# Optimization experiments

Hardware: AMD Instinct MI355X
Metric: run time of the kernel (lower is better)

The kernel has to match this reference:

```python
import jax, jax.numpy as jnp
import numpy as np

K = 1000   # grid rows (detections from model 1, truncated to 1000)
N = 1000   # grid cols (detections from model 2)
M = 900000 # number of non-empty (overlapping) pairs
F = 7      # per-pair feature dim
SENTINEL = -9999.0


def setup_inputs() -> dict:
    key = jax.random.key(0)
    ks = jax.random.split(key, 12)
    def w(k, o, i):
        return jax.random.normal(k, (o, i), dtype=jnp.float32) * 0.05
    def b(k, o):
        return jax.random.normal(k, (o,), dtype=jnp.float32) * 0.05
    return {
        "input_1": jax.random.normal(ks[0], (1, F, 1, M), dtype=jnp.float32),
        "T_out": jnp.zeros((1, K, N), dtype=jnp.float32),
        "T_indices": jax.random.randint(ks[1], (2, M), 0, K),
        "w1": w(ks[2], 18, F),  "b1": b(ks[3], 18),
        "w2": w(ks[4], 36, 18), "b2": b(ks[5], 36),
        "w3": w(ks[6], 36, 36), "b3": b(ks[7], 36),
        "w4": w(ks[8], 1, 36),  "b4": b(ks[9], 1),
    }


def reference(input_1, T_out, T_indices, w1, b1, w2, b2, w3, b3, w4, b4):
    # 1x1 conv stack == channel matmuls on the flattened [F, M] features.
    x = input_1[0, :, 0, :]                       # [F, M]
    h = jax.nn.relu(w1 @ x + b1[:, None])         # [18, M]
    h = jax.nn.relu(w2 @ h + b2[:, None])         # [36, M]
    h = jax.nn.relu(w3 @ h + b3[:, None])         # [36, M]
    vals = (w4 @ h + b4[:, None])[0]              # [M]

    grid = jnp.full(T_out.shape, SENTINEL, dtype=T_out.dtype)  # [1, K, N]
    grid = grid.at[:, T_indices[0], T_indices[1]].set(vals[None, :])

    # MaxPool2d([1, N]) -> max over cols; MaxPool2d([K, 1]) -> max over rows.
    row_max = grid.max(axis=2).squeeze()          # [K]
    col_max = grid.max(axis=1).squeeze()          # [N]
    return (row_max, col_max)
```

## Files before the change

### kernel.cpp

```cpp
#include <hip/hip_runtime.h>
#include <stdint.h>

#define KK 1000
#define NN 1000
#define MM 900000
#define FF 7
#define SENTINEL -9999.0f

#define R18(X) X(0) X(1) X(2) X(3) X(4) X(5) X(6) X(7) X(8) X(9) X(10) X(11) \
               X(12) X(13) X(14) X(15) X(16) X(17)
#define R36(X) R18(X) X(18) X(19) X(20) X(21) X(22) X(23) X(24) X(25) X(26) \
               X(27) X(28) X(29) X(30) X(31) X(32) X(33) X(34) X(35)

__global__ __launch_bounds__(256) void init_grid(ulonglong2* __restrict__ g, int n2) {
    int i = blockIdx.x * 256 + threadIdx.x;
    if (i < n2) g[i] = make_ulonglong2(0ULL, 0ULL);
}

__global__ __launch_bounds__(256, 4) void mlp_scatter(
    const float* __restrict__ in,
    const int*   __restrict__ idx,
    const float* __restrict__ w1, const float* __restrict__ b1,
    const float* __restrict__ w2, const float* __restrict__ b2,
    const float* __restrict__ w3, const float* __restrict__ b3,
    const float* __restrict__ w4, const float* __restrict__ b4,
    unsigned long long* __restrict__ grid)
{
    int m0 = blockIdx.x * 256 + threadIdx.x;
    int m = m0 < MM ? m0 : (MM - 1);

    float x0 = in[0 * MM + m], x1 = in[1 * MM + m], x2 = in[2 * MM + m],
          x3 = in[3 * MM + m], x4 = in[4 * MM + m], x5 = in[5 * MM + m],
          x6 = in[6 * MM + m];

#define L1(o) float h1_##o; { float a = b1[o];                                 \
    a = fmaf(w1[(o)*7+0], x0, a); a = fmaf(w1[(o)*7+1], x1, a);                \
    a = fmaf(w1[(o)*7+2], x2, a); a = fmaf(w1[(o)*7+3], x3, a);                \
    a = fmaf(w1[(o)*7+4], x4, a); a = fmaf(w1[(o)*7+5], x5, a);                \
    a = fmaf(w1[(o)*7+6], x6, a); h1_##o = fmaxf(a, 0.0f); }
    R18(L1)
#undef L1

#define L2(o) float h2_##o; { float a = b2[o];                                 \
    a = fmaf(w2[(o)*18+ 0], h1_0,  a); a = fmaf(w2[(o)*18+ 1], h1_1,  a);      \
    a = fmaf(w2[(o)*18+ 2], h1_2,  a); a = fmaf(w2[(o)*18+ 3], h1_3,  a);      \
    a = fmaf(w2[(o)*18+ 4], h1_4,  a); a = fmaf(w2[(o)*18+ 5], h1_5,  a);      \
    a = fmaf(w2[(o)*18+ 6], h1_6,  a); a = fmaf(w2[(o)*18+ 7], h1_7,  a);      \
    a = fmaf(w2[(o)*18+ 8], h1_8,  a); a = fmaf(w2[(o)*18+ 9], h1_9,  a);      \
    a = fmaf(w2[(o)*18+10], h1_10, a); a = fmaf(w2[(o)*18+11], h1_11, a);      \
    a = fmaf(w2[(o)*18+12], h1_12, a); a = fmaf(w2[(o)*18+13], h1_13, a);      \
    a = fmaf(w2[(o)*18+14], h1_14, a); a = fmaf(w2[(o)*18+15], h1_15, a);      \
    a = fmaf(w2[(o)*18+16], h1_16, a); a = fmaf(w2[(o)*18+17], h1_17, a);      \
    h2_##o = fmaxf(a, 0.0f); }
    R36(L2)
#undef L2

    float v = b4[0];
#define L34(o) { float a = b3[o];                                              \
    a = fmaf(w3[(o)*36+ 0], h2_0,  a); a = fmaf(w3[(o)*36+ 1], h2_1,  a);      \
    a = fmaf(w3[(o)*36+ 2], h2_2,  a); a = fmaf(w3[(o)*36+ 3], h2_3,  a);      \
    a = fmaf(w3[(o)*36+ 4], h2_4,  a); a = fmaf(w3[(o)*36+ 5], h2_5,  a);      \
    a = fmaf(w3[(o)*36+ 6], h2_6,  a); a = fmaf(w3[(o)*36+ 7], h2_7,  a);      \
    a = fmaf(w3[(o)*36+ 8], h2_8,  a); a = fmaf(w3[(o)*36+ 9], h2_9,  a);      \
    a = fmaf(w3[(o)*36+10], h2_10, a); a = fmaf(w3[(o)*36+11], h2_11, a);      \
    a = fmaf(w3[(o)*36+12], h2_12, a); a = fmaf(w3[(o)*36+13], h2_13, a);      \
    a = fmaf(w3[(o)*36+14], h2_14, a); a = fmaf(w3[(o)*36+15], h2_15, a);      \
    a = fmaf(w3[(o)*36+16], h2_16, a); a = fmaf(w3[(o)*36+17], h2_17, a);      \
    a = fmaf(w3[(o)*36+18], h2_18, a); a = fmaf(w3[(o)*36+19], h2_19, a);      \
    a = fmaf(w3[(o)*36+20], h2_20, a); a = fmaf(w3[(o)*36+21], h2_21, a);      \
    a = fmaf(w3[(o)*36+22], h2_22, a); a = fmaf(w3[(o)*36+23], h2_23, a);      \
    a = fmaf(w3[(o)*36+24], h2_24, a); a = fmaf(w3[(o)*36+25], h2_25, a);      \
    a = fmaf(w3[(o)*36+26], h2_26, a); a = fmaf(w3[(o)*36+27], h2_27, a);      \
    a = fmaf(w3[(o)*36+28], h2_28, a); a = fmaf(w3[(o)*36+29], h2_29, a);      \
    a = fmaf(w3[(o)*36+30], h2_30, a); a = fmaf(w3[(o)*36+31], h2_31, a);      \
    a = fmaf(w3[(o)*36+32], h2_32, a); a = fmaf(w3[(o)*36+33], h2_33, a);      \
    a = fmaf(w3[(o)*36+34], h2_34, a); a = fmaf(w3[(o)*36+35], h2_35, a);      \
    v = fmaf(w4[o], fmaxf(a, 0.0f), v); }
    R36(L34)
#undef L34

    int r = idx[m];
    int c = idx[MM + m];
    unsigned long long packed =
        ((unsigned long long)(unsigned)(m + 1) << 32) | (unsigned)__float_as_uint(v);
    atomicMax(&grid[r * NN + c], packed);
}

__global__ __launch_bounds__(256) void row_max_k(const unsigned long long* __restrict__ g,
                                                 float* __restrict__ out) {
    int r = blockIdx.x;
    float mx = SENTINEL;
    for (int c = threadIdx.x; c < NN; c += 256) {
        unsigned long long p = g[(size_t)r * NN + c];
        if (p) mx = fmaxf(mx, __uint_as_float((unsigned)p));
    }
    __shared__ float red[256];
    red[threadIdx.x] = mx;
    __syncthreads();
    for (int s = 128; s > 0; s >>= 1) {
        if (threadIdx.x < s) red[threadIdx.x] = fmaxf(red[threadIdx.x], red[threadIdx.x + s]);
        __syncthreads();
    }
    if (threadIdx.x == 0) out[r] = red[0];
}

#define CCHUNKS 25
#define CROWS   (KK / CCHUNKS)

__global__ __launch_bounds__(256) void col_partial(const unsigned long long* __restrict__ g,
                                                   float* __restrict__ part) {
    int n = blockIdx.x * 256 + threadIdx.x;
    if (n >= NN) return;
    int k0 = blockIdx.y * CROWS;
    float mx = SENTINEL;
    for (int k = k0; k < k0 + CROWS; ++k) {
        unsigned long long p = g[(size_t)k * NN + n];
        if (p) mx = fmaxf(mx, __uint_as_float((unsigned)p));
    }
    part[blockIdx.y * NN + n] = mx;
}

__global__ __launch_bounds__(256) void col_final(const float* __restrict__ part,
                                                 float* __restrict__ out) {
    int n = blockIdx.x * 256 + threadIdx.x;
    if (n >= NN) return;
    float mx = SENTINEL;
#pragma unroll
    for (int c = 0; c < CCHUNKS; ++c) mx = fmaxf(mx, part[c * NN + n]);
    out[KK + n] = mx;
}

extern "C" void kernel_launch(void* const* d_in, const int* in_sizes, int n_in,
                              void* d_out, int out_size, void* d_ws, size_t ws_size,
                              hipStream_t stream) {
    const float* in  = (const float*)d_in[0];
    const int*   idx = (const int*)d_in[2];
    const float* w1  = (const float*)d_in[3];
    const float* b1  = (const float*)d_in[4];
    const float* w2  = (const float*)d_in[5];
    const float* b2  = (const float*)d_in[6];
    const float* w3  = (const float*)d_in[7];
    const float* b3  = (const float*)d_in[8];
    const float* w4  = (const float*)d_in[9];
    const float* b4  = (const float*)d_in[10];

    unsigned long long* grid = (unsigned long long*)d_ws;
    float* part = (float*)((char*)d_ws + (size_t)KK * NN * 8);
    float* out  = (float*)d_out;

    const int n2 = (KK * NN) / 2;
    init_grid<<<(n2 + 255) / 256, 256, 0, stream>>>((ulonglong2*)grid, n2);

    mlp_scatter<<<(MM + 255) / 256, 256, 0, stream>>>(
        in, idx, w1, b1, w2, b2, w3, b3, w4, b4, grid);

    row_max_k<<<KK, 256, 0, stream>>>(grid, out);
    col_partial<<<dim3(4, CCHUNKS), 256, 0, stream>>>(grid, part);
    col_final<<<4, 256, 0, stream>>>(part, out);
}
```

Before: 176.2 us.

## Fuse row and column max into one grid pass; load MLP weights via constant address space

Replaces the separate row-max and column-partial kernels with one kernel in which each block reads 10 rows once, producing per-row maxima through wave shuffles and per-column partial maxima for 100 row chunks. This means the 8 MB grid is read once instead of twice and one launch is removed. The MLP weight pointers are also cast to address space 4 (constant), so the compiler can use scalar loads for the uniform weights. The cost is fewer reduction blocks (100) and a col_final that now loops over 100 partials instead of 25.

```diff
diff --git a/kernel.cpp b/kernel.cpp
--- a/kernel.cpp
+++ b/kernel.cpp
@@ -6,6 +6,8 @@
 #define MM 900000
 #define FF 7
 #define SENTINEL -9999.0f
+
+#define AS4 __attribute__((address_space(4)))
 
 #define R18(X) X(0) X(1) X(2) X(3) X(4) X(5) X(6) X(7) X(8) X(9) X(10) X(11) \
                X(12) X(13) X(14) X(15) X(16) X(17)
@@ -20,12 +22,21 @@
 __global__ __launch_bounds__(256, 4) void mlp_scatter(
     const float* __restrict__ in,
     const int*   __restrict__ idx,
-    const float* __restrict__ w1, const float* __restrict__ b1,
-    const float* __restrict__ w2, const float* __restrict__ b2,
-    const float* __restrict__ w3, const float* __restrict__ b3,
-    const float* __restrict__ w4, const float* __restrict__ b4,
+    const float* __restrict__ w1p, const float* __restrict__ b1p,
+    const float* __restrict__ w2p, const float* __restrict__ b2p,
+    const float* __restrict__ w3p, const float* __restrict__ b3p,
+    const float* __restrict__ w4p, const float* __restrict__ b4p,
     unsigned long long* __restrict__ grid)
 {
+    const AS4 float* w1 = (const AS4 float*)w1p;
+    const AS4 float* b1 = (const AS4 float*)b1p;
+    const AS4 float* w2 = (const AS4 float*)w2p;
+    const AS4 float* b2 = (const AS4 float*)b2p;
+    const AS4 float* w3 = (const AS4 float*)w3p;
+    const AS4 float* b3 = (const AS4 float*)b3p;
+    const AS4 float* w4 = (const AS4 float*)w4p;
+    const AS4 float* b4 = (const AS4 float*)b4p;
+
     int m0 = blockIdx.x * 256 + threadIdx.x;
     int m = m0 < MM ? m0 : (MM - 1);
 
@@ -86,38 +97,50 @@
     atomicMax(&grid[r * NN + c], packed);
 }
 
-__global__ __launch_bounds__(256) void row_max_k(const unsigned long long* __restrict__ g,
-                                                 float* __restrict__ out) {
-    int r = blockIdx.x;
-    float mx = SENTINEL;
-    for (int c = threadIdx.x; c < NN; c += 256) {
-        unsigned long long p = g[(size_t)r * NN + c];
-        if (p) mx = fmaxf(mx, __uint_as_float((unsigned)p));
-    }
-    __shared__ float red[256];
-    red[threadIdx.x] = mx;
-    __syncthreads();
-    for (int s = 128; s > 0; s >>= 1) {
-        if (threadIdx.x < s) red[threadIdx.x] = fmaxf(red[threadIdx.x], red[threadIdx.x + s]);
+#define RPB     10
+#define NBLK    (KK / RPB)
+
+__global__ __launch_bounds__(256) void reduce_grid(const unsigned long long* __restrict__ g,
+                                                   float* __restrict__ out,
+                                                   float* __restrict__ part)
+{
+    int tid = threadIdx.x;
+    int r0  = blockIdx.x * RPB;
+    float cmax0 = SENTINEL, cmax1 = SENTINEL, cmax2 = SENTINEL, cmax3 = SENTINEL;
+    __shared__ float red[4];
+
+    for (int rr = 0; rr < RPB; ++rr) {
+        int r = r0 + rr;
+        const unsigned long long* row = g + (size_t)r * NN;
+        float rmax = SENTINEL;
+        {
+            unsigned long long p = row[tid];
+            if (p) { float val = __uint_as_float((unsigned)p); rmax = fmaxf(rmax, val); cmax0 = fmaxf(cmax0, val); }
+        }
+        {
+            unsigned long long p = row[tid + 256];
+            if (p) { float val = __uint_as_float((unsigned)p); rmax = fmaxf(rmax, val); cmax1 = fmaxf(cmax1, val); }
+        }
+        {
+            unsigned long long p = row[tid + 512];
+            if (p) { float val = __uint_as_float((unsigned)p); rmax = fmaxf(rmax, val); cmax2 = fmaxf(cmax2, val); }
+        }
+        if (tid < NN - 768) {
+            unsigned long long p = row[tid + 768];
+            if (p) { float val = __uint_as_float((unsigned)p); rmax = fmaxf(rmax, val); cmax3 = fmaxf(cmax3, val); }
+        }
+        for (int s = 32; s > 0; s >>= 1) rmax = fmaxf(rmax, __shfl_down(rmax, s, 64));
+        if ((tid & 63) == 0) red[tid >> 6] = rmax;
+        __syncthreads();
+        if (tid == 0) out[r] = fmaxf(fmaxf(red[0], red[1]), fmaxf(red[2], red[3]));
         __syncthreads();
     }
-    if (threadIdx.x == 0) out[r] = red[0];
-}
 
-#define CCHUNKS 25
-#define CROWS   (KK / CCHUNKS)
-
-__global__ __launch_bounds__(256) void col_partial(const unsigned long long* __restrict__ g,
-                                                   float* __restrict__ part) {
-    int n = blockIdx.x * 256 + threadIdx.x;
-    if (n >= NN) return;
-    int k0 = blockIdx.y * CROWS;
-    float mx = SENTINEL;
-    for (int k = k0; k < k0 + CROWS; ++k) {
-        unsigned long long p = g[(size_t)k * NN + n];
-        if (p) mx = fmaxf(mx, __uint_as_float((unsigned)p));
-    }
-    part[blockIdx.y * NN + n] = mx;
+    float* p = part + (size_t)blockIdx.x * NN;
+    p[tid]       = cmax0;
+    p[tid + 256] = cmax1;
+    p[tid + 512] = cmax2;
+    if (tid < NN - 768) p[tid + 768] = cmax3;
 }
 
 __global__ __launch_bounds__(256) void col_final(const float* __restrict__ part,
@@ -125,8 +148,7 @@
     int n = blockIdx.x * 256 + threadIdx.x;
     if (n >= NN) return;
     float mx = SENTINEL;
-#pragma unroll
-    for (int c = 0; c < CCHUNKS; ++c) mx = fmaxf(mx, part[c * NN + n]);
+    for (int c = 0; c < NBLK; ++c) mx = fmaxf(mx, part[c * NN + n]);
     out[KK + n] = mx;
 }
 
@@ -154,7 +176,6 @@
     mlp_scatter<<<(MM + 255) / 256, 256, 0, stream>>>(
         in, idx, w1, b1, w2, b2, w3, b3, w4, b4, grid);
 
-    row_max_k<<<KK, 256, 0, stream>>>(grid, out);
-    col_partial<<<dim3(4, CCHUNKS), 256, 0, stream>>>(grid, part);
+    reduce_grid<<<NBLK, 256, 0, stream>>>(grid, out, part);
     col_final<<<4, 256, 0, stream>>>(part, out);
 }
```

Result: slower. 194.5 us (+10.4%).
